# Kernel tuning notes

Measured on AMD Instinct MI355X. Metric: run time of the kernel, lower is better.

Reference implementation:

```python
import jax, jax.numpy as jnp
import numpy as np

ALPHA = 0.1   # erase strength (module default scalar path)
BETA = 1.0    # write strength
EPS = 1e-12   # F.normalize eps


def setup_inputs() -> dict:
    key = jax.random.key(0)
    k1, k2 = jax.random.split(key)
    T, DK, DV, H = 8192, 1024, 1024, 8
    return {
        "k": jax.random.normal(k1, (T, DK), dtype=jnp.float32),
        "v": jax.random.normal(k2, (T, DV), dtype=jnp.float32),
        "W0": jnp.zeros((H, DK, DV), dtype=jnp.float32),  # module registers W as zeros
    }


def reference(k, v, W0):
    # k: [T, d_k], v: [T, d_v], W0: [h, d_k, d_v]
    # Each step t (Nested Learning Eq. 114):
    #   retrieved_t = einsum('hkv,k->hv', W, k_t)            (read BEFORE update)
    #   W <- W @ (I - alpha k k^T) + beta k v^T
    # Algebraically identical rank-1 form (avoids the O(h*d_k^2) erase mask):
    #   W <- W + k \otimes (beta*v - alpha*retrieved)
    kn = k / jnp.maximum(jnp.linalg.norm(k, axis=-1, keepdims=True), EPS)

    def step(W, kv):
        kt, vt = kv                                   # kt: [d_k], vt: [d_v]
        r = jnp.einsum('hkv,k->hv', W, kt)            # retrieved per head [h, d_v]
        W_new = W + kt[None, :, None] * (BETA * vt[None, None, :] - ALPHA * r[:, None, :])
        return W_new, r.mean(axis=0)                  # mean over heads -> [d_v]

    _, outs = jax.lax.scan(step, W0, (kn, v))
    return outs  # [T, d_v]: retrieved value before each update
```

## Files before the change

### kernel.cpp

```cpp
#include <hip/hip_runtime.h>
#include <hip/hip_bf16.h>


#define T_   8192
#define DKC  1024
#define DVC  1024
#define C_   32
#define NC   (T_ / C_)
#define JB   4
#define NB   (DVC / JB)
#define ALPHA_ 0.1f

#define K3_S4O   32768
#define K3_RPO   36928
#define K3_WLO   39056
#define K3_VLO   39184
#define K3_ULO   39312
#define K3_SMEM_FLOATS 39440
#define K3_SMEM_BYTES  (K3_SMEM_FLOATS * 4)

#define K2_KNC   0
#define K2_A     32896
#define K2_ML    33952
#define K2_SMEM_BYTES  (35008 * 4)

template <int CTRL>
__device__ __forceinline__ float qadd(float x) {
    return x + __int_as_float(__builtin_amdgcn_mov_dpp(__float_as_int(x), CTRL, 0xF, 0xF, true));
}
__device__ __forceinline__ float qsum(float x) {
    return qadd<0x4E>(qadd<0xB1>(x));
}
__device__ __forceinline__ float sel4(int L, float a, float b, float c, float d) {
    float r = (L == 1) ? b : a;
    r = (L == 2) ? c : r;
    r = (L == 3) ? d : r;
    return r;
}

#define FULLBAR() do { asm volatile("s_waitcnt lgkmcnt(0)" ::: "memory"); \
                       __builtin_amdgcn_s_barrier(); \
                       asm volatile("" ::: "memory"); } while (0)
#define TOPBAR()  do { asm volatile("s_waitcnt vmcnt(8) lgkmcnt(0)" ::: "memory"); \
                       __builtin_amdgcn_s_barrier(); \
                       asm volatile("" ::: "memory"); } while (0)
#define VBAR0()   do { asm volatile("s_waitcnt vmcnt(0) lgkmcnt(0)" ::: "memory"); \
                       __builtin_amdgcn_s_barrier(); \
                       asm volatile("" ::: "memory"); } while (0)

extern "C" __global__ __launch_bounds__(256)
void k1_norm(const float* __restrict__ k, float* __restrict__ kn) {
    __shared__ float red[4];
    __shared__ float sInv;
    const int row = blockIdx.x, tid = threadIdx.x;
    float4 v = ((const float4*)k)[(size_t)row * 256 + tid];
    float ss = v.x * v.x + v.y * v.y + v.z * v.z + v.w * v.w;
    for (int off = 32; off > 0; off >>= 1) ss += __shfl_down(ss, off, 64);
    if ((tid & 63) == 0) red[tid >> 6] = ss;
    __syncthreads();
    if (tid == 0) {
        float s = red[0] + red[1] + red[2] + red[3];
        sInv = 1.0f / fmaxf(sqrtf(s), 1e-12f);
    }
    __syncthreads();
    const float inv = sInv;
    float4 o; o.x = v.x * inv; o.y = v.y * inv; o.z = v.z * inv; o.w = v.w * inv;
    ((float4*)kn)[(size_t)row * 256 + tid] = o;
}

extern "C" __global__ __launch_bounds__(256)
void k2_gram(const float* __restrict__ kn, float* __restrict__ Mg) {
    extern __shared__ float smem[];
    float4* KnC = (float4*)(smem + K2_KNC);
    float*  A   = smem + K2_A;
    float*  Ml  = smem + K2_ML;
    const int tid = threadIdx.x, c = blockIdx.x, base = c * C_;
    const float4* kn4 = (const float4*)kn;

    for (int m = 0; m < 32; ++m) {
        int n = m * 256 + tid;
        int t = n >> 8, k4 = n & 255;
        KnC[t * 257 + k4] = kn4[(size_t)(base + t) * 256 + k4];
    }
    __syncthreads();

    for (int m = 0; m < 4; ++m) {
        int o = m * 256 + tid;
        int i = o >> 5, p = o & 31;
        const float4* ri = KnC + i * 257;
        const float4* rp = KnC + p * 257;
        float ax = 0.f, ay = 0.f, az = 0.f, aw = 0.f;
        for (int kk = 0; kk < 256; ++kk) {
            float4 a = ri[kk], b = rp[kk];
            ax += a.x * b.x; ay += a.y * b.y; az += a.z * b.z; aw += a.w * b.w;
        }
        A[i * 33 + p] = (ax + ay) + (az + aw);
    }
    __syncthreads();

    if (tid < 32) {
        const int j = tid;
        for (int i = 0; i < 32; ++i) {
            float acc = 0.f;
            for (int p = 0; p < i; ++p) acc += A[i * 33 + p] * Ml[p * 33 + j];
            Ml[i * 33 + j] = (i == j ? 1.0f : 0.0f) - ALPHA_ * acc;
        }
    }
    __syncthreads();

    for (int n = tid; n < 1024; n += 256)
        Mg[(size_t)c * 1024 + n] = Ml[(n >> 5) * 33 + (n & 31)];
}

#define FMA44(R_, KF_) \
    acc[R_][0].x += KF_.x*sf0.x; acc[R_][0].y += KF_.y*sf0.y; acc[R_][0].z += KF_.z*sf0.z; acc[R_][0].w += KF_.w*sf0.w; \
    acc[R_][1].x += KF_.x*sf1.x; acc[R_][1].y += KF_.y*sf1.y; acc[R_][1].z += KF_.z*sf1.z; acc[R_][1].w += KF_.w*sf1.w; \
    acc[R_][2].x += KF_.x*sf2.x; acc[R_][2].y += KF_.y*sf2.y; acc[R_][2].z += KF_.z*sf2.z; acc[R_][2].w += KF_.w*sf2.w; \
    acc[R_][3].x += KF_.x*sf3.x; acc[R_][3].y += KF_.y*sf3.y; acc[R_][3].z += KF_.z*sf3.z; acc[R_][3].w += KF_.w*sf3.w;

#define B_STEP(S_) do { \
    const int k4_ = ln + 64*(S_); \
    float4 kf0 = KnL[(wv4+0)*256 + k4_]; \
    float4 kf1 = KnL[(wv4+1)*256 + k4_]; \
    float4 kf2 = KnL[(wv4+2)*256 + k4_]; \
    float4 kf3 = KnL[(wv4+3)*256 + k4_]; \
    float4 sf0 = S4v[0*260 + k4_]; \
    float4 sf1 = S4v[1*260 + k4_]; \
    float4 sf2 = S4v[2*260 + k4_]; \
    float4 sf3 = S4v[3*260 + k4_]; \
    FMA44(0, kf0) FMA44(1, kf1) FMA44(2, kf2) FMA44(3, kf3) \
  } while (0)

#define STAGE_HALF(C_, H_) do { \
    _Pragma("unroll") \
    for (int m_ = 0; m_ < 8; ++m_) { \
      const int idx_ = wv*8 + m_; \
      const int f4i_ = (idx_ >> 1)*256 + (H_)*128 + (idx_ & 1)*64; \
      __builtin_amdgcn_global_load_lds( \
        (const __attribute__((address_space(1))) unsigned int*)(kn4 + (size_t)(C_)*8192 + f4i_ + ln), \
        (__attribute__((address_space(3))) unsigned int*)(KnL + f4i_), \
        16, 0, 0); \
    } \
  } while (0)

#define D_HALF(H_) do { \
    float4 aj0, aj1, aj2, aj3; \
    aj0.x=aj0.y=aj0.z=aj0.w=0.f; aj1.x=aj1.y=aj1.z=aj1.w=0.f; \
    aj2.x=aj2.y=aj2.z=aj2.w=0.f; aj3.x=aj3.y=aj3.z=aj3.w=0.f; \
    _Pragma("unroll") \
    for (int ii = 0; ii < 8; ++ii) { \
      float4 kf = KnL[(ig*8 + ii)*256 + (H_)*128 + kb]; \
      aj0.x += kf.x*uf[ii].x; aj0.y += kf.y*uf[ii].x; aj0.z += kf.z*uf[ii].x; aj0.w += kf.w*uf[ii].x; \
      aj1.x += kf.x*uf[ii].y; aj1.y += kf.y*uf[ii].y; aj1.z += kf.z*uf[ii].y; aj1.w += kf.w*uf[ii].y; \
      aj2.x += kf.x*uf[ii].z; aj2.y += kf.y*uf[ii].z; aj2.z += kf.z*uf[ii].z; aj2.w += kf.w*uf[ii].z; \
      aj3.x += kf.x*uf[ii].w; aj3.y += kf.y*uf[ii].w; aj3.z += kf.z*uf[ii].w; aj3.w += kf.w*uf[ii].w; \
    } \
    aj0.x = qsum(aj0.x); aj0.y = qsum(aj0.y); aj0.z = qsum(aj0.z); aj0.w = qsum(aj0.w); \
    aj1.x = qsum(aj1.x); aj1.y = qsum(aj1.y); aj1.z = qsum(aj1.z); aj1.w = qsum(aj1.w); \
    aj2.x = qsum(aj2.x); aj2.y = qsum(aj2.y); aj2.z = qsum(aj2.z); aj2.w = qsum(aj2.w); \
    aj3.x = qsum(aj3.x); aj3.y = qsum(aj3.y); aj3.z = qsum(aj3.z); aj3.w = qsum(aj3.w); \
    float4 mine; \
    mine.x = sel4(ig, aj0.x, aj1.x, aj2.x, aj3.x); \
    mine.y = sel4(ig, aj0.y, aj1.y, aj2.y, aj3.y); \
    mine.z = sel4(ig, aj0.z, aj1.z, aj2.z, aj3.z); \
    mine.w = sel4(ig, aj0.w, aj1.w, aj2.w, aj3.w); \
    float4* sp = &S4v[ig*260 + (H_)*128 + kb]; \
    float4 s_ = *sp; \
    s_.x += mine.x; s_.y += mine.y; s_.z += mine.z; s_.w += mine.w; \
    *sp = s_; \
  } while (0)

extern "C" __global__ __launch_bounds__(512, 1)
void k3_main(const float* __restrict__ kn, const float* __restrict__ v,
             const float* __restrict__ Mg, float* __restrict__ out) {
    extern __shared__ float smem[];
    float4* KnL = (float4*)smem;
    float4* S4v = (float4*)(smem + K3_S4O);
    float*  Rp  = smem + K3_RPO;
    float*  Wl  = smem + K3_WLO;
    float*  Vl  = smem + K3_VLO;
    float*  Ul  = smem + K3_ULO;

    const int tid = threadIdx.x;
    const int wv  = tid >> 6;
    const int wv4 = wv * 4;
    const int ln  = tid & 63;
    const int kb  = tid >> 2;
    const int ig  = tid & 3;
    const int colbase = blockIdx.x * JB;

    const float4* kn4 = (const float4*)kn;

    { float4 z; z.x = z.y = z.z = z.w = 0.f;
      for (int n = tid; n < 1040; n += 512) S4v[n] = z; }

    STAGE_HALF(0, 0);
    STAGE_HALF(0, 1);

    for (int c = 0; c < NC; ++c) {
        const int base = c * C_;

        TOPBAR();

        float vreg = 0.f;
        if ((tid & 3) == 0)
            vreg = v[(size_t)(base + (tid >> 4)) * DVC + colbase + ((tid >> 2) & 3)];

        float4 acc[4][4];
        #pragma unroll
        for (int r = 0; r < 4; ++r)
            #pragma unroll
            for (int j = 0; j < 4; ++j) { acc[r][j].x = acc[r][j].y = acc[r][j].z = acc[r][j].w = 0.f; }

        B_STEP(0); B_STEP(1);
        VBAR0();
        B_STEP(2); B_STEP(3);

        float red[4][4];
        #pragma unroll
        for (int r = 0; r < 4; ++r)
            #pragma unroll
            for (int j = 0; j < 4; ++j) {
                float4 a = acc[r][j];
                red[r][j] = qsum((a.x + a.y) + (a.z + a.w));
            }
        {
            const int quad = ln >> 2, L = ln & 3;
            const int obase = quad * 133 + (wv4 << 2);
            #pragma unroll
            for (int j = 0; j < 4; ++j) {
                float w = sel4(L, red[0][j], red[1][j], red[2][j], red[3][j]);
                Rp[obase + (L << 2) + j] = w;
            }
        }
        FULLBAR();

        {
            const int o = tid >> 2, q4 = tid & 3;
            const int rb = q4 * 4 * 133 + o;
            float s0 = Rp[rb], s1 = Rp[rb + 133], s2 = Rp[rb + 266], s3 = Rp[rb + 399];
            float rs = qsum((s0 + s1) + (s2 + s3));
            if (q4 == 0) { Wl[o] = vreg - ALPHA_ * rs; Vl[o] = vreg; }
        }
        FULLBAR();

        if (tid < 128) {
            const int i = tid >> 2, pq = tid & 3;
            const float* mrow = Mg + (size_t)c * 1024 + i * 32 + pq * 8;
            float4 m0 = *(const float4*)mrow;
            float4 m1 = *(const float4*)(mrow + 4);
            float mm[8] = {m0.x, m0.y, m0.z, m0.w, m1.x, m1.y, m1.z, m1.w};
            const float4* wl4 = (const float4*)Wl;
            float4 a; a.x = a.y = a.z = a.w = 0.f;
            #pragma unroll
            for (int kk = 0; kk < 8; ++kk) {
                float4 wf = wl4[pq * 8 + kk];
                a.x += mm[kk] * wf.x; a.y += mm[kk] * wf.y;
                a.z += mm[kk] * wf.z; a.w += mm[kk] * wf.w;
            }
            a.x = qsum(a.x); a.y = qsum(a.y); a.z = qsum(a.z); a.w = qsum(a.w);
            if (pq == 0) {
                ((float4*)Ul)[i] = a;
                float4 V = ((const float4*)Vl)[i];
                float4 o4;
                o4.x = (V.x - a.x) * 10.f; o4.y = (V.y - a.y) * 10.f;
                o4.z = (V.z - a.z) * 10.f; o4.w = (V.w - a.w) * 10.f;
                *(float4*)&out[(size_t)(base + i) * DVC + colbase] = o4;
            }
        }
        FULLBAR();

        float4 uf[8];
        #pragma unroll
        for (int ii = 0; ii < 8; ++ii) uf[ii] = ((const float4*)Ul)[ig * 8 + ii];

        D_HALF(0);
        FULLBAR();
        if (c + 1 < NC) STAGE_HALF(c + 1, 0);
        D_HALF(1);
        FULLBAR();
        if (c + 1 < NC) STAGE_HALF(c + 1, 1);
    }
}

extern "C" void kernel_launch(void* const* d_in, const int* in_sizes, int n_in,
                              void* d_out, int out_size, void* d_ws, size_t ws_size,
                              hipStream_t stream) {
    const float* k = (const float*)d_in[0];
    const float* v = (const float*)d_in[1];
    float* out = (float*)d_out;

    float* kn = (float*)d_ws;
    float* Mg = kn + (size_t)T_ * DKC;

    (void)hipFuncSetAttribute((const void*)k2_gram,
            hipFuncAttributeMaxDynamicSharedMemorySize, K2_SMEM_BYTES);
    (void)hipFuncSetAttribute((const void*)k3_main,
            hipFuncAttributeMaxDynamicSharedMemorySize, K3_SMEM_BYTES);

    k1_norm<<<T_, 256, 0, stream>>>(k, kn);
    k2_gram<<<NC, 256, K2_SMEM_BYTES, stream>>>(kn, Mg);
    k3_main<<<NB, 512, K3_SMEM_BYTES, stream>>>(kn, v, Mg, out);
}
```

Baseline: 1.581 ms.

## Swizzle Kn LDS layout to cut bank conflicts and parallelize U solve over all threads

Applies an XOR swizzle to the chunk's normalized-key tile in LDS, both when staging via global_load_lds and in the B-step and D-step reads, to reduce LDS bank conflicts. The W-to-U triangular multiply now runs on all 512 threads using a transposed W buffer instead of 128 threads. It also drops the separate V buffer by reusing the per-thread v register when writing output. The swizzle has to stay consistent across the staging, B-step, D-step and U buffer indexing, which risks correctness if any index is wrong.

```diff
diff --git a/kernel.cpp b/kernel.cpp
--- a/kernel.cpp
+++ b/kernel.cpp
@@ -13,10 +13,9 @@
 
 #define K3_S4O   32768
 #define K3_RPO   36928
-#define K3_WLO   39056
-#define K3_VLO   39184
-#define K3_ULO   39312
-#define K3_SMEM_FLOATS 39440
+#define K3_WLTO  39056
+#define K3_ULO   39200
+#define K3_SMEM_FLOATS 39328
 #define K3_SMEM_BYTES  (K3_SMEM_FLOATS * 4)
 
 #define K2_KNC   0
@@ -120,10 +119,11 @@
 
 #define B_STEP(S_) do { \
     const int k4_ = ln + 64*(S_); \
-    float4 kf0 = KnL[(wv4+0)*256 + k4_]; \
-    float4 kf1 = KnL[(wv4+1)*256 + k4_]; \
-    float4 kf2 = KnL[(wv4+2)*256 + k4_]; \
-    float4 kf3 = KnL[(wv4+3)*256 + k4_]; \
+    const int k4x_ = k4_ ^ szw;     \
+    float4 kf0 = KnL[(wv4+0)*256 + k4x_]; \
+    float4 kf1 = KnL[(wv4+1)*256 + k4x_]; \
+    float4 kf2 = KnL[(wv4+2)*256 + k4x_]; \
+    float4 kf3 = KnL[(wv4+3)*256 + k4x_]; \
     float4 sf0 = S4v[0*260 + k4_]; \
     float4 sf1 = S4v[1*260 + k4_]; \
     float4 sf2 = S4v[2*260 + k4_]; \
@@ -135,9 +135,11 @@
     _Pragma("unroll") \
     for (int m_ = 0; m_ < 8; ++m_) { \
       const int idx_ = wv*8 + m_; \
-      const int f4i_ = (idx_ >> 1)*256 + (H_)*128 + (idx_ & 1)*64; \
+      const int row_ = idx_ >> 1; \
+      const int szr_ = ((row_ >> 3) & 3) << 1; \
+      const int f4i_ = row_*256 + (H_)*128 + (idx_ & 1)*64; \
       __builtin_amdgcn_global_load_lds( \
-        (const __attribute__((address_space(1))) unsigned int*)(kn4 + (size_t)(C_)*8192 + f4i_ + ln), \
+        (const __attribute__((address_space(1))) unsigned int*)(kn4 + (size_t)(C_)*8192 + f4i_ + (ln ^ szr_)), \
         (__attribute__((address_space(3))) unsigned int*)(KnL + f4i_), \
         16, 0, 0); \
     } \
@@ -149,7 +151,7 @@
     aj2.x=aj2.y=aj2.z=aj2.w=0.f; aj3.x=aj3.y=aj3.z=aj3.w=0.f; \
     _Pragma("unroll") \
     for (int ii = 0; ii < 8; ++ii) { \
-      float4 kf = KnL[(ig*8 + ii)*256 + (H_)*128 + kb]; \
+      float4 kf = KnL[(ig*8 + ii)*256 + (H_)*128 + kbx];  \
       aj0.x += kf.x*uf[ii].x; aj0.y += kf.y*uf[ii].x; aj0.z += kf.z*uf[ii].x; aj0.w += kf.w*uf[ii].x; \
       aj1.x += kf.x*uf[ii].y; aj1.y += kf.y*uf[ii].y; aj1.z += kf.z*uf[ii].y; aj1.w += kf.w*uf[ii].y; \
       aj2.x += kf.x*uf[ii].z; aj2.y += kf.y*uf[ii].z; aj2.z += kf.z*uf[ii].z; aj2.w += kf.w*uf[ii].z; \
@@ -177,16 +179,17 @@
     float4* KnL = (float4*)smem;
     float4* S4v = (float4*)(smem + K3_S4O);
     float*  Rp  = smem + K3_RPO;
-    float*  Wl  = smem + K3_WLO;
-    float*  Vl  = smem + K3_VLO;
+    float*  Wlt = smem + K3_WLTO;
     float*  Ul  = smem + K3_ULO;
 
     const int tid = threadIdx.x;
     const int wv  = tid >> 6;
     const int wv4 = wv * 4;
     const int ln  = tid & 63;
+    const int szw = ((wv4 >> 3) & 3) << 1;
     const int kb  = tid >> 2;
     const int ig  = tid & 3;
+    const int kbx = kb ^ (ig << 1);
     const int colbase = blockIdx.x * JB;
 
     const float4* kn4 = (const float4*)kn;
@@ -240,39 +243,32 @@
             const int rb = q4 * 4 * 133 + o;
             float s0 = Rp[rb], s1 = Rp[rb + 133], s2 = Rp[rb + 266], s3 = Rp[rb + 399];
             float rs = qsum((s0 + s1) + (s2 + s3));
-            if (q4 == 0) { Wl[o] = vreg - ALPHA_ * rs; Vl[o] = vreg; }
-        }
-        FULLBAR();
-
-        if (tid < 128) {
-            const int i = tid >> 2, pq = tid & 3;
-            const float* mrow = Mg + (size_t)c * 1024 + i * 32 + pq * 8;
-            float4 m0 = *(const float4*)mrow;
-            float4 m1 = *(const float4*)(mrow + 4);
-            float mm[8] = {m0.x, m0.y, m0.z, m0.w, m1.x, m1.y, m1.z, m1.w};
-            const float4* wl4 = (const float4*)Wl;
-            float4 a; a.x = a.y = a.z = a.w = 0.f;
-            #pragma unroll
-            for (int kk = 0; kk < 8; ++kk) {
-                float4 wf = wl4[pq * 8 + kk];
-                a.x += mm[kk] * wf.x; a.y += mm[kk] * wf.y;
-                a.z += mm[kk] * wf.z; a.w += mm[kk] * wf.w;
-            }
-            a.x = qsum(a.x); a.y = qsum(a.y); a.z = qsum(a.z); a.w = qsum(a.w);
+            if (q4 == 0) Wlt[(o & 3) * 36 + (o >> 2)] = vreg - ALPHA_ * rs;
+        }
+        FULLBAR();
+
+        {
+            const int i  = tid >> 4;
+            const int j  = (tid >> 2) & 3;
+            const int pq = tid & 3;
+            const float4* mrow4 = (const float4*)(Mg + (size_t)c * 1024 + i * 32 + pq * 8);
+            float4 m0 = mrow4[0], m1 = mrow4[1];
+            const float4* wrow4 = (const float4*)(Wlt + j * 36 + pq * 8);
+            float4 w0 = wrow4[0], w1 = wrow4[1];
+            float u = m0.x*w0.x + m0.y*w0.y + m0.z*w0.z + m0.w*w0.w
+                    + m1.x*w1.x + m1.y*w1.y + m1.z*w1.z + m1.w*w1.w;
+            u = qsum(u);
             if (pq == 0) {
-                ((float4*)Ul)[i] = a;
-                float4 V = ((const float4*)Vl)[i];
-                float4 o4;
-                o4.x = (V.x - a.x) * 10.f; o4.y = (V.y - a.y) * 10.f;
-                o4.z = (V.z - a.z) * 10.f; o4.w = (V.w - a.w) * 10.f;
-                *(float4*)&out[(size_t)(base + i) * DVC + colbase] = o4;
+                Ul[((i ^ ((i >> 3) << 1)) << 2) + j] = u;
+                out[(size_t)(base + i) * DVC + colbase + j] = (vreg - u) * 10.0f;
             }
         }
         FULLBAR();
 
         float4 uf[8];
         #pragma unroll
-        for (int ii = 0; ii < 8; ++ii) uf[ii] = ((const float4*)Ul)[ig * 8 + ii];
+        for (int ii = 0; ii < 8; ++ii)
+            uf[ii] = ((const float4*)Ul)[(ig * 8 + ii) ^ (ig << 1)];
 
         D_HALF(0);
         FULLBAR();
```

New measurement: 1.504 ms. 1.05x faster.
